# Performance work log

Hardware: AMD Instinct MI355X
Metric: run time of the kernel (lower is better)

## Reference

```python
import jax, jax.numpy as jnp
import numpy as np

D_MODEL = 1536
NUM_EXPERTS = 64
TOP_K = 2
D_HIDDEN = 512
LN_EPS = 1e-5


def setup_inputs() -> dict:
    key = jax.random.key(0)
    ks = jax.random.split(key, 6)
    B, S = 2, 2048
    x = jax.random.normal(ks[0], (B, S, D_MODEL), dtype=jnp.float32)
    # router: nn.Linear(d_model, num_experts, bias=False) -> weight [E, D]
    Wr = jax.random.normal(ks[1], (NUM_EXPERTS, D_MODEL), dtype=jnp.float32) / np.sqrt(D_MODEL)
    # per-expert MLP weights, torch Linear layout: w1 [H, D], w2 [D, H], stacked over experts
    W1 = jax.random.normal(ks[2], (NUM_EXPERTS, D_HIDDEN, D_MODEL), dtype=jnp.float32) / np.sqrt(D_MODEL)
    W2 = jax.random.normal(ks[3], (NUM_EXPERTS, D_MODEL, D_HIDDEN), dtype=jnp.float32) / np.sqrt(D_HIDDEN)
    gamma = jnp.ones((D_MODEL,), dtype=jnp.float32)
    beta = jnp.zeros((D_MODEL,), dtype=jnp.float32)
    return {"x": x, "Wr": Wr, "W1": W1, "W2": W2, "gamma": gamma, "beta": beta}


def reference(x, Wr, W1, W2, gamma, beta):
    B, S, D = x.shape
    xf = x.reshape(-1, D)                                   # [T, D]
    logits = xf @ Wr.T                                      # [T, E]
    top_w, top_idx = jax.lax.top_k(logits, TOP_K)           # [T, K]
    top_w = jax.nn.softmax(top_w, axis=-1)                  # softmax over selected k
    # combine[t, e] = sum_k top_w[t, k] * 1{top_idx[t,k]==e}; zero for unselected experts,
    # so dense all-expert compute below is mathematically identical to the masked loop.
    onehot = jax.nn.one_hot(top_idx, NUM_EXPERTS, dtype=xf.dtype)   # [T, K, E]
    combine = jnp.einsum("tk,tke->te", top_w, onehot)       # [T, E]
    h = jax.nn.silu(jnp.einsum("td,ehd->teh", xf, W1))      # [T, E, H]
    hw = h * combine[:, :, None]                            # weight before second GEMM
    out = jnp.einsum("teh,edh->td", hw, W2)                 # [T, D]
    # LayerNorm (eps=1e-5, affine)
    mu = jnp.mean(out, axis=-1, keepdims=True)
    var = jnp.mean(jnp.square(out - mu), axis=-1, keepdims=True)
    out = (out - mu) * jax.lax.rsqrt(var + LN_EPS) * gamma + beta
    return out.reshape(B, S, D)
```

## Files before the change

kernel.cpp:

```cpp
#include <hip/hip_runtime.h>
#include <hip/hip_bf16.h>

#define D_MODEL 1536
#define NEXP    64
#define D_HID   512
#define NTOK    4096
#define NT1     (D_MODEL / 64)
#define NT2     (D_HID / 64)
#define MT      192

typedef __attribute__((ext_vector_type(8))) short short8;
typedef __attribute__((ext_vector_type(4))) float f32x4;

__device__ __forceinline__ unsigned short f2bf(float f) {
  unsigned u = __builtin_bit_cast(unsigned, f);
  u += 0x7FFFu + ((u >> 16) & 1u);
  return (unsigned short)(u >> 16);
}
__device__ __forceinline__ unsigned pk2(float a, float b) {
  return (unsigned)f2bf(a) | ((unsigned)f2bf(b) << 16);
}
__device__ __forceinline__ float bf2f(unsigned short u) {
  return __builtin_bit_cast(float, ((unsigned)u) << 16);
}

__device__ __forceinline__ void gl16(const void* g, void* s) {
  __builtin_amdgcn_global_load_lds(
      (const __attribute__((address_space(1))) unsigned int*)g,
      (__attribute__((address_space(3))) unsigned int*)s, 16, 0, 0);
}

#define WAITV(N)  asm volatile("s_waitcnt vmcnt(" #N ")" ::: "memory")
#define WAITL0    asm volatile("s_waitcnt lgkmcnt(0)" ::: "memory")
#define SBAR      __builtin_amdgcn_s_barrier()
#define SCHED0    __builtin_amdgcn_sched_barrier(0)


__global__ void zero_small_kernel(int* __restrict__ counts) {
  counts[threadIdx.x] = 0;
}


__global__ __launch_bounds__(256) void cvt_split_kernel(const float* __restrict__ x,
    const float* __restrict__ Wr,
    unsigned short* __restrict__ xhi, unsigned short* __restrict__ xlo,
    unsigned short* __restrict__ whi, unsigned short* __restrict__ wlo)
{
  const float* src; unsigned short* dhi; unsigned short* dlo; long i;
  long bid = blockIdx.x;
  if (bid < 3072) { src = x;  dhi = xhi; dlo = xlo; i = (bid * 256 + threadIdx.x) * 8; }
  else            { src = Wr; dhi = whi; dlo = wlo; i = ((bid - 3072) * 256 + threadIdx.x) * 8; }
  float4 a = *(const float4*)(src + i);
  float4 b = *(const float4*)(src + i + 4);
  float f[8] = {a.x, a.y, a.z, a.w, b.x, b.y, b.z, b.w};
  unsigned short h[8], l[8];
  #pragma unroll
  for (int j = 0; j < 8; ++j) {
    h[j] = f2bf(f[j]);
    l[j] = f2bf(f[j] - bf2f(h[j]));
  }
  uint4 ph, pl;
  ph.x = (unsigned)h[0] | ((unsigned)h[1] << 16);
  ph.y = (unsigned)h[2] | ((unsigned)h[3] << 16);
  ph.z = (unsigned)h[4] | ((unsigned)h[5] << 16);
  ph.w = (unsigned)h[6] | ((unsigned)h[7] << 16);
  pl.x = (unsigned)l[0] | ((unsigned)l[1] << 16);
  pl.y = (unsigned)l[2] | ((unsigned)l[3] << 16);
  pl.z = (unsigned)l[4] | ((unsigned)l[5] << 16);
  pl.w = (unsigned)l[6] | ((unsigned)l[7] << 16);
  *(uint4*)(dhi + i) = ph;
  *(uint4*)(dlo + i) = pl;
}


__global__ __launch_bounds__(256) void router_kernel(
    const unsigned short* __restrict__ xhi, const unsigned short* __restrict__ xlo,
    const unsigned short* __restrict__ whi, const unsigned short* __restrict__ wlo,
    int* __restrict__ topidx, float* __restrict__ topw, int* __restrict__ counts)
{
  __shared__ unsigned short lds[8 * 4096];
  const int tid  = threadIdx.x;
  const int lane = tid & 63;
  const int wv   = tid >> 6;
  const int t0   = blockIdx.x * 64;

  const int lslot = (lane & 7) ^ (lane >> 3);
  const unsigned short* gsrc[4][2];
  #pragma unroll
  for (int j = 0; j < 2; ++j) {
    int r = (wv * 2 + j) * 8 + (lane >> 3);
    gsrc[0][j] = xhi + (long)(t0 + r) * D_MODEL + lslot * 8;
    gsrc[1][j] = xlo + (long)(t0 + r) * D_MODEL + lslot * 8;
    gsrc[2][j] = whi + (long)r * D_MODEL + lslot * 8;
    gsrc[3][j] = wlo + (long)r * D_MODEL + lslot * 8;
  }

  auto ISSUE = [&](int t, int b) {
    const int k0 = t * 64;
    SCHED0;
    #pragma unroll
    for (int tile = 0; tile < 4; ++tile)
      #pragma unroll
      for (int j = 0; j < 2; ++j)
        gl16(gsrc[tile][j] + k0, &lds[(b * 4 + tile) * 4096 + (wv * 2 + j) * 512]);
    SCHED0;
  };

  f32x4 acc[4];
  #pragma unroll
  for (int i = 0; i < 4; ++i) acc[i] = (f32x4)0.f;

  const int arow = wv * 16 + (lane & 15);

  auto COMPUTE = [&](int b) {
    const unsigned short* Ah = &lds[(b * 4 + 0) * 4096];
    const unsigned short* Al = &lds[(b * 4 + 1) * 4096];
    const unsigned short* Bh = &lds[(b * 4 + 2) * 4096];
    const unsigned short* Bl = &lds[(b * 4 + 3) * 4096];
    #pragma unroll
    for (int ks = 0; ks < 2; ++ks) {
      int pa = (ks * 4 + (lane >> 4)) ^ (arow & 7);
      short8 ah = *(const short8*)(Ah + arow * 64 + pa * 8);
      short8 al = *(const short8*)(Al + arow * 64 + pa * 8);
      short8 bh[4], bl[4];
      #pragma unroll
      for (int ni = 0; ni < 4; ++ni) {
        int br = ni * 16 + (lane & 15);
        int pb = (ks * 4 + (lane >> 4)) ^ (br & 7);
        bh[ni] = *(const short8*)(Bh + br * 64 + pb * 8);
        bl[ni] = *(const short8*)(Bl + br * 64 + pb * 8);
      }
      __builtin_amdgcn_s_setprio(1);
      #pragma unroll
      for (int ni = 0; ni < 4; ++ni) {
        acc[ni] = __builtin_amdgcn_mfma_f32_16x16x32_bf16(ah, bh[ni], acc[ni], 0, 0, 0);
        acc[ni] = __builtin_amdgcn_mfma_f32_16x16x32_bf16(ah, bl[ni], acc[ni], 0, 0, 0);
        acc[ni] = __builtin_amdgcn_mfma_f32_16x16x32_bf16(al, bh[ni], acc[ni], 0, 0, 0);
      }
      __builtin_amdgcn_s_setprio(0);
    }
  };

  ISSUE(0, 0);
  ISSUE(1, 1);
  WAITV(8);
  SBAR;

  #pragma unroll 1
  for (int t = 0; t < NT1; t += 2) {
    COMPUTE(0);
    SBAR;
    if (t + 2 < NT1) { ISSUE(t + 2, 0); WAITV(8); }
    else             { WAITV(0); }
    SBAR;
    COMPUTE(1);
    SBAR;
    if (t + 2 < NT1) {
      if (t + 3 < NT1) { ISSUE(t + 3, 1); WAITV(8); }
      else             { WAITV(0); }
      SBAR;
    }
  }

  float* lgl = (float*)lds;
  #pragma unroll
  for (int ni = 0; ni < 4; ++ni)
    #pragma unroll
    for (int rg = 0; rg < 4; ++rg) {
      int tok = wv * 16 + (lane >> 4) * 4 + rg;
      int e   = ni * 16 + (lane & 15);
      lgl[tok * 66 + e] = acc[ni][rg];
    }
  __syncthreads();

  for (int i = 0; i < 16; ++i) {
    const int tl = wv * 16 + i;
    float v = lgl[tl * 66 + lane];
    float v0 = v; int e0 = lane;
    #pragma unroll
    for (int off = 32; off > 0; off >>= 1) {
      float ov = __shfl_xor(v0, off);
      int   oe = __shfl_xor(e0, off);
      if (ov > v0 || (ov == v0 && oe < e0)) { v0 = ov; e0 = oe; }
    }
    float v1 = (lane == e0) ? -3.0e38f : v;
    int e1 = lane;
    #pragma unroll
    for (int off = 32; off > 0; off >>= 1) {
      float ov = __shfl_xor(v1, off);
      int   oe = __shfl_xor(e1, off);
      if (ov > v1 || (ov == v1 && oe < e1)) { v1 = ov; e1 = oe; }
    }
    if (lane == 0) {
      int tt = t0 + tl;
      float w0 = 1.f / (1.f + expf(v1 - v0));
      topidx[tt * 2]     = e0;
      topidx[tt * 2 + 1] = e1;
      topw[tt * 2]       = w0;
      topw[tt * 2 + 1]   = 1.f - w0;
      atomicAdd(&counts[e0], 1);
      atomicAdd(&counts[e1], 1);
    }
  }
}


__global__ void scan_kernel(const int* __restrict__ counts, int* __restrict__ offs,
                            int* __restrict__ cursor)
{
  int e = threadIdx.x;
  int c = counts[e];
  int xx = c;
  #pragma unroll
  for (int off = 1; off < 64; off <<= 1) {
    int y = __shfl_up(xx, off);
    if (e >= off) xx += y;
  }
  offs[e + 1] = xx;
  if (e == 0) offs[0] = 0;
  cursor[e] = 0;
}

__global__ void scatter_kernel(const int* __restrict__ topidx, const float* __restrict__ topw,
    const int* __restrict__ offs, int* __restrict__ cursor,
    int* __restrict__ perm, float* __restrict__ wgt, int* __restrict__ tok2slot)
{
  int t = blockIdx.x * blockDim.x + threadIdx.x;
  if (t >= NTOK) return;
  #pragma unroll
  for (int k = 0; k < 2; ++k) {
    int e = topidx[t * 2 + k];
    float w = topw[t * 2 + k];
    int pos = atomicAdd(&cursor[e], 1);
    int slot = offs[e] + pos;
    perm[slot] = t;
    wgt[slot] = w;
    tok2slot[t * 2 + k] = slot;
  }
}


__global__ __launch_bounds__(256, 2) void ffn1_kernel(
    const unsigned short* __restrict__ xb, const float* __restrict__ W1,
    const int* __restrict__ offs, const int* __restrict__ perm,
    const float* __restrict__ wgt, unsigned short* __restrict__ hbuf)
{
  const int nc = blockIdx.x;
  const int e  = blockIdx.y;
  const int cnt = offs[e + 1] - offs[e];
  if (cnt == 0) return;

  __shared__ unsigned short Abuf[2][MT * 64];
  __shared__ unsigned short Bbuf[2][64 * 64];

  const int tid  = threadIdx.x;
  const int lane = tid & 63;
  const int wv   = tid >> 6;

  const int qB = tid & 15;
  const int rB = tid >> 4;
  const float* bptr[4];
  #pragma unroll
  for (int p = 0; p < 4; ++p)
    bptr[p] = W1 + ((long)e * D_HID + nc * 64 + p * 16 + rB) * D_MODEL + qB * 4;

  int arow[3], brow[4];
  int physA[2][3], physB[2][4];
  #pragma unroll
  for (int mi = 0; mi < 3; ++mi) {
    arow[mi] = wv * 48 + mi * 16 + (lane & 15);
    #pragma unroll
    for (int ks = 0; ks < 2; ++ks)
      physA[ks][mi] = (ks * 4 + (lane >> 4)) ^ (arow[mi] & 7);
  }
  #pragma unroll
  for (int ni = 0; ni < 4; ++ni) {
    brow[ni] = ni * 16 + (lane & 15);
    #pragma unroll
    for (int ks = 0; ks < 2; ++ks)
      physB[ks][ni] = (ks * 4 + (lane >> 4)) ^ (brow[ni] & 7);
  }
  const int lslot = (lane & 7) ^ (lane >> 3);

  for (int m0 = 0; m0 < cnt; m0 += MT) {
    const int base = offs[e] + m0;
    const int mcnt = min(MT, cnt - m0);

    const unsigned short* gptrA[6];
    #pragma unroll
    for (int j = 0; j < 6; ++j) {
      int pr = (wv * 6 + j) * 8 + (lane >> 3);
      if (pr >= mcnt) pr = mcnt - 1;
      gptrA[j] = xb + (long)perm[base + pr] * D_MODEL + lslot * 8;
    }

    f32x4 acc[3][4];
    #pragma unroll
    for (int i = 0; i < 3; ++i)
      #pragma unroll
      for (int j = 0; j < 4; ++j) acc[i][j] = (f32x4)0.f;

    float4 bregA[4], bregB[4];

    auto ISSUE = [&](int t, float4* br, unsigned short* Ab) {
      const int k0 = t * 64;
      SCHED0;
      #pragma unroll
      for (int p = 0; p < 4; ++p) br[p] = *(const float4*)(bptr[p] + k0);
      SCHED0;
      #pragma unroll
      for (int j = 0; j < 6; ++j)
        gl16(gptrA[j] + k0, Ab + (wv * 6 + j) * 512);
      SCHED0;
    };
    auto WRITE_B = [&](const float4* br, unsigned short* B_) {
      #pragma unroll
      for (int p = 0; p < 4; ++p) {
        int rr = p * 16 + rB;
        unsigned lo = pk2(br[p].x, br[p].y);
        unsigned hi = pk2(br[p].z, br[p].w);
        int ph = (qB >> 1) ^ (rr & 7);
        *(uint2*)(B_ + rr * 64 + ph * 8 + (qB & 1) * 4) = make_uint2(lo, hi);
      }
    };
    auto COMPUTE = [&](const unsigned short* A_, const unsigned short* B_) {
      #pragma unroll
      for (int ks = 0; ks < 2; ++ks) {
        short8 a[3], bb[4];
        #pragma unroll
        for (int mi = 0; mi < 3; ++mi)
          a[mi] = *(const short8*)(A_ + arow[mi] * 64 + physA[ks][mi] * 8);
        #pragma unroll
        for (int ni = 0; ni < 4; ++ni)
          bb[ni] = *(const short8*)(B_ + brow[ni] * 64 + physB[ks][ni] * 8);
        __builtin_amdgcn_s_setprio(1);
        #pragma unroll
        for (int mi = 0; mi < 3; ++mi)
          #pragma unroll
          for (int ni = 0; ni < 4; ++ni)
            acc[mi][ni] = __builtin_amdgcn_mfma_f32_16x16x32_bf16(a[mi], bb[ni], acc[mi][ni], 0, 0, 0);
        __builtin_amdgcn_s_setprio(0);
      }
    };

    ISSUE(0, bregA, Abuf[0]);
    WAITV(6);
    WRITE_B(bregA, Bbuf[0]);
    ISSUE(1, bregB, Abuf[1]);
    WAITV(10);
    WAITL0;
    SBAR;

    #pragma unroll 1
    for (int t = 0; t < NT1; t += 2) {
      COMPUTE(Abuf[0], Bbuf[0]);
      SBAR;
      WAITV(6);
      WRITE_B(bregB, Bbuf[1]);
      if (t + 2 < NT1) { ISSUE(t + 2, bregA, Abuf[0]); WAITV(10); }
      else             { WAITV(0); }
      WAITL0;
      SBAR;
      COMPUTE(Abuf[1], Bbuf[1]);
      SBAR;
      if (t + 2 < NT1) {
        WAITV(6);
        WRITE_B(bregA, Bbuf[0]);
        if (t + 3 < NT1) { ISSUE(t + 3, bregB, Abuf[1]); WAITV(10); }
        else             { WAITV(0); }
        WAITL0;
        SBAR;
      }
    }

    unsigned short* fds = &Abuf[0][0];
    const int rsub = (lane >> 4) * 4;
    const int csub = lane & 15;
    #pragma unroll
    for (int mi = 0; mi < 3; ++mi) {
      #pragma unroll
      for (int rg = 0; rg < 4; ++rg) {
        int r = wv * 48 + mi * 16 + rsub + rg;
        float wt = (r < mcnt) ? wgt[base + r] : 0.f;
        #pragma unroll
        for (int ni = 0; ni < 4; ++ni) {
          float v = acc[mi][ni][rg];
          float sv = v / (1.f + __expf(-v)) * wt;
          fds[r * 64 + ni * 16 + csub] = f2bf(sv);
        }
      }
    }
    __syncthreads();
    #pragma unroll
    for (int q = 0; q < 6; ++q) {
      int idx = q * 256 + tid;
      int row = idx >> 3, c8 = idx & 7;
      if (row < mcnt)
        *(uint4*)(hbuf + (long)(base + row) * D_HID + nc * 64 + c8 * 8) =
            *(const uint4*)(fds + row * 64 + c8 * 8);
    }
    __syncthreads();
  }
}


__global__ __launch_bounds__(256, 2) void ffn2_kernel(
    const unsigned short* __restrict__ hbuf, const float* __restrict__ W2,
    const int* __restrict__ offs, unsigned short* __restrict__ sbuf)
{
  const int nc = blockIdx.x;
  const int e  = blockIdx.y;
  const int cnt = offs[e + 1] - offs[e];
  if (cnt == 0) return;

  __shared__ unsigned short Abuf[2][MT * 64];
  __shared__ unsigned short Bbuf[2][64 * 64];

  const int tid  = threadIdx.x;
  const int lane = tid & 63;
  const int wv   = tid >> 6;

  const int qB = tid & 15;
  const int rB = tid >> 4;
  const float* bptr[4];
  #pragma unroll
  for (int p = 0; p < 4; ++p)
    bptr[p] = W2 + ((long)e * D_MODEL + nc * 64 + p * 16 + rB) * D_HID + qB * 4;

  int arow[3], brow[4];
  int physA[2][3], physB[2][4];
  #pragma unroll
  for (int mi = 0; mi < 3; ++mi) {
    arow[mi] = wv * 48 + mi * 16 + (lane & 15);
    #pragma unroll
    for (int ks = 0; ks < 2; ++ks)
      physA[ks][mi] = (ks * 4 + (lane >> 4)) ^ (arow[mi] & 7);
  }
  #pragma unroll
  for (int ni = 0; ni < 4; ++ni) {
    brow[ni] = ni * 16 + (lane & 15);
    #pragma unroll
    for (int ks = 0; ks < 2; ++ks)
      physB[ks][ni] = (ks * 4 + (lane >> 4)) ^ (brow[ni] & 7);
  }
  const int lslot = (lane & 7) ^ (lane >> 3);

  for (int m0 = 0; m0 < cnt; m0 += MT) {
    const int base = offs[e] + m0;
    const int mcnt = min(MT, cnt - m0);

    const unsigned short* gptrA[6];
    #pragma unroll
    for (int j = 0; j < 6; ++j) {
      int pr = (wv * 6 + j) * 8 + (lane >> 3);
      if (pr >= mcnt) pr = mcnt - 1;
      gptrA[j] = hbuf + (long)(base + pr) * D_HID + lslot * 8;
    }

    f32x4 acc[3][4];
    #pragma unroll
    for (int i = 0; i < 3; ++i)
      #pragma unroll
      for (int j = 0; j < 4; ++j) acc[i][j] = (f32x4)0.f;

    float4 bregA[4], bregB[4];

    auto ISSUE = [&](int t, float4* br, unsigned short* Ab) {
      const int k0 = t * 64;
      SCHED0;
      #pragma unroll
      for (int p = 0; p < 4; ++p) br[p] = *(const float4*)(bptr[p] + k0);
      SCHED0;
      #pragma unroll
      for (int j = 0; j < 6; ++j)
        gl16(gptrA[j] + k0, Ab + (wv * 6 + j) * 512);
      SCHED0;
    };
    auto WRITE_B = [&](const float4* br, unsigned short* B_) {
      #pragma unroll
      for (int p = 0; p < 4; ++p) {
        int rr = p * 16 + rB;
        unsigned lo = pk2(br[p].x, br[p].y);
        unsigned hi = pk2(br[p].z, br[p].w);
        int ph = (qB >> 1) ^ (rr & 7);
        *(uint2*)(B_ + rr * 64 + ph * 8 + (qB & 1) * 4) = make_uint2(lo, hi);
      }
    };
    auto COMPUTE = [&](const unsigned short* A_, const unsigned short* B_) {
      #pragma unroll
      for (int ks = 0; ks < 2; ++ks) {
        short8 a[3], bb[4];
        #pragma unroll
        for (int mi = 0; mi < 3; ++mi)
          a[mi] = *(const short8*)(A_ + arow[mi] * 64 + physA[ks][mi] * 8);
        #pragma unroll
        for (int ni = 0; ni < 4; ++ni)
          bb[ni] = *(const short8*)(B_ + brow[ni] * 64 + physB[ks][ni] * 8);
        __builtin_amdgcn_s_setprio(1);
        #pragma unroll
        for (int mi = 0; mi < 3; ++mi)
          #pragma unroll
          for (int ni = 0; ni < 4; ++ni)
            acc[mi][ni] = __builtin_amdgcn_mfma_f32_16x16x32_bf16(a[mi], bb[ni], acc[mi][ni], 0, 0, 0);
        __builtin_amdgcn_s_setprio(0);
      }
    };

    ISSUE(0, bregA, Abuf[0]);
    WAITV(6);
    WRITE_B(bregA, Bbuf[0]);
    ISSUE(1, bregB, Abuf[1]);
    WAITV(10);
    WAITL0;
    SBAR;

    #pragma unroll 1
    for (int t = 0; t < NT2; t += 2) {
      COMPUTE(Abuf[0], Bbuf[0]);
      SBAR;
      WAITV(6);
      WRITE_B(bregB, Bbuf[1]);
      if (t + 2 < NT2) { ISSUE(t + 2, bregA, Abuf[0]); WAITV(10); }
      else             { WAITV(0); }
      WAITL0;
      SBAR;
      COMPUTE(Abuf[1], Bbuf[1]);
      SBAR;
      if (t + 2 < NT2) {
        WAITV(6);
        WRITE_B(bregA, Bbuf[0]);
        if (t + 3 < NT2) { ISSUE(t + 3, bregB, Abuf[1]); WAITV(10); }
        else             { WAITV(0); }
        WAITL0;
        SBAR;
      }
    }

    unsigned short* fds = &Abuf[0][0];
    const int rsub = (lane >> 4) * 4;
    const int csub = lane & 15;
    #pragma unroll
    for (int mi = 0; mi < 3; ++mi) {
      #pragma unroll
      for (int rg = 0; rg < 4; ++rg) {
        int r = wv * 48 + mi * 16 + rsub + rg;
        #pragma unroll
        for (int ni = 0; ni < 4; ++ni)
          fds[r * 64 + ni * 16 + csub] = f2bf(acc[mi][ni][rg]);
      }
    }
    __syncthreads();
    #pragma unroll
    for (int q = 0; q < 6; ++q) {
      int idx = q * 256 + tid;
      int row = idx >> 3, c8 = idx & 7;
      if (row < mcnt)
        *(uint4*)(sbuf + (long)(base + row) * D_MODEL + nc * 64 + c8 * 8) =
            *(const uint4*)(fds + row * 64 + c8 * 8);
    }
    __syncthreads();
  }
}


__global__ __launch_bounds__(192) void ln_kernel(const unsigned short* __restrict__ sbuf,
    const int* __restrict__ tok2slot, float* __restrict__ out,
    const float* __restrict__ gamma, const float* __restrict__ beta)
{
  const int tid = threadIdx.x;
  const int t = blockIdx.x;
  const long r0 = (long)tok2slot[t * 2]     * D_MODEL;
  const long r1 = (long)tok2slot[t * 2 + 1] * D_MODEL;

  uint4 u0 = *(const uint4*)(sbuf + r0 + tid * 8);
  uint4 u1 = *(const uint4*)(sbuf + r1 + tid * 8);
  float v[8];
  {
    const unsigned* p0 = &u0.x;
    const unsigned* p1 = &u1.x;
    #pragma unroll
    for (int i = 0; i < 4; ++i) {
      v[i * 2]     = bf2f((unsigned short)(p0[i] & 0xFFFFu)) + bf2f((unsigned short)(p1[i] & 0xFFFFu));
      v[i * 2 + 1] = bf2f((unsigned short)(p0[i] >> 16))     + bf2f((unsigned short)(p1[i] >> 16));
    }
  }

  float s = 0.f, sq = 0.f;
  #pragma unroll
  for (int i = 0; i < 8; ++i) { s += v[i]; sq += v[i] * v[i]; }
  #pragma unroll
  for (int off = 32; off > 0; off >>= 1) {
    s  += __shfl_xor(s, off);
    sq += __shfl_xor(sq, off);
  }
  __shared__ float ss[3], sqs[3];
  int wv = tid >> 6;
  if ((tid & 63) == 0) { ss[wv] = s; sqs[wv] = sq; }
  __syncthreads();
  s  = ss[0] + ss[1] + ss[2];
  sq = sqs[0] + sqs[1] + sqs[2];
  const float inv = 1.f / (float)D_MODEL;
  float mu  = s * inv;
  float var = sq * inv - mu * mu;
  float rs  = 1.f / sqrtf(var + 1e-5f);

  float4 g1 = *(const float4*)(gamma + tid * 8);
  float4 g2 = *(const float4*)(gamma + tid * 8 + 4);
  float4 b1v = *(const float4*)(beta + tid * 8);
  float4 b2v = *(const float4*)(beta + tid * 8 + 4);
  float4 a, b;
  a.x = (v[0] - mu) * rs * g1.x + b1v.x;
  a.y = (v[1] - mu) * rs * g1.y + b1v.y;
  a.z = (v[2] - mu) * rs * g1.z + b1v.z;
  a.w = (v[3] - mu) * rs * g1.w + b1v.w;
  b.x = (v[4] - mu) * rs * g2.x + b2v.x;
  b.y = (v[5] - mu) * rs * g2.y + b2v.y;
  b.z = (v[6] - mu) * rs * g2.z + b2v.z;
  b.w = (v[7] - mu) * rs * g2.w + b2v.w;
  float* row = out + (long)t * D_MODEL;
  *(float4*)(row + tid * 8)     = a;
  *(float4*)(row + tid * 8 + 4) = b;
}


extern "C" void kernel_launch(void* const* d_in, const int* in_sizes, int n_in,
                              void* d_out, int out_size, void* d_ws, size_t ws_size,
                              hipStream_t stream) {
  const float* x     = (const float*)d_in[0];
  const float* Wr    = (const float*)d_in[1];
  const float* W1    = (const float*)d_in[2];
  const float* W2    = (const float*)d_in[3];
  const float* gamma = (const float*)d_in[4];
  const float* beta  = (const float*)d_in[5];
  float* out = (float*)d_out;

  char* ws = (char*)d_ws;
  unsigned short* xhi    = (unsigned short*)(ws + 0);
  unsigned short* xlo    = (unsigned short*)(ws + 12582912);
  unsigned short* hbuf   = (unsigned short*)(ws + 25165824);
  unsigned short* sbuf   = (unsigned short*)(ws + 33554432);
  unsigned short* whi    = (unsigned short*)(ws + 58720256);
  unsigned short* wlo    = (unsigned short*)(ws + 58916864);
  int*   topidx   = (int*)  (ws + 59113472);
  float* topw     = (float*)(ws + 59146240);
  int*   counts   = (int*)  (ws + 59179008);
  int*   cursor   = (int*)  (ws + 59179264);
  int*   offs     = (int*)  (ws + 59179520);
  int*   tok2slot = (int*)  (ws + 59180032);
  int*   perm     = (int*)  (ws + 59212800);
  float* wgt      = (float*)(ws + 59245568);

  hipLaunchKernelGGL(zero_small_kernel, dim3(1), dim3(64), 0, stream, counts);
  hipLaunchKernelGGL(cvt_split_kernel, dim3(3120), dim3(256), 0, stream, x, Wr, xhi, xlo, whi, wlo);
  hipLaunchKernelGGL(router_kernel, dim3(NTOK / 64), dim3(256), 0, stream, xhi, xlo, whi, wlo, topidx, topw, counts);
  hipLaunchKernelGGL(scan_kernel, dim3(1), dim3(64), 0, stream, counts, offs, cursor);
  hipLaunchKernelGGL(scatter_kernel, dim3(NTOK / 256), dim3(256), 0, stream, topidx, topw, offs, cursor, perm, wgt, tok2slot);
  hipLaunchKernelGGL(ffn1_kernel, dim3(8, NEXP), dim3(256), 0, stream, xhi, W1, offs, perm, wgt, hbuf);
  hipLaunchKernelGGL(ffn2_kernel, dim3(24, NEXP), dim3(256), 0, stream, hbuf, W2, offs, sbuf);
  hipLaunchKernelGGL(ln_kernel, dim3(NTOK), dim3(192), 0, stream, sbuf, tok2slot, out, gamma, beta);
}
```

Baseline: 217.9 us.

## Deepen B-operand prefetch to three register stages in expert FFN GEMMs

New measurement: 220.6 us. About the same (+1.2%).

```diff
diff --git a/kernel.cpp b/kernel.cpp
--- a/kernel.cpp
+++ b/kernel.cpp
@@ -239,6 +239,19 @@
   }
 }
 
+#define FS(T, AB, BRI, BRW, KNT)                                   \
+  {                                                                \
+    COMPUTE(Abuf[AB], Bbuf[AB]);                                   \
+    SBAR;                                                          \
+    if ((T) + 2 < (KNT)) ISSUEA((T) + 2, Abuf[AB]);                \
+    if ((T) + 3 < (KNT)) ISSUEB((T) + 3, BRI);                     \
+    if ((T) + 3 < (KNT))      { WAITV(14); }                       \
+    else if ((T) + 2 < (KNT)) { WAITV(10); }                       \
+    else                      { WAITV(0);  }                       \
+    if ((T) + 1 < (KNT)) { WRITE_B(BRW, Bbuf[(AB) ^ 1]); WAITL0; } \
+    SBAR;                                                          \
+  }
+
 
 __global__ __launch_bounds__(256, 2) void ffn1_kernel(
     const unsigned short* __restrict__ xb, const float* __restrict__ W1,
@@ -300,17 +313,21 @@
       #pragma unroll
       for (int j = 0; j < 4; ++j) acc[i][j] = (f32x4)0.f;
 
-    float4 bregA[4], bregB[4];
-
-    auto ISSUE = [&](int t, float4* br, unsigned short* Ab) {
+    float4 br0[4], br1[4], br2[4];
+
+    auto ISSUEA = [&](int t, unsigned short* Ab) {
       const int k0 = t * 64;
-      SCHED0;
-      #pragma unroll
-      for (int p = 0; p < 4; ++p) br[p] = *(const float4*)(bptr[p] + k0);
       SCHED0;
       #pragma unroll
       for (int j = 0; j < 6; ++j)
         gl16(gptrA[j] + k0, Ab + (wv * 6 + j) * 512);
+      SCHED0;
+    };
+    auto ISSUEB = [&](int t, float4* br) {
+      const int k0 = t * 64;
+      SCHED0;
+      #pragma unroll
+      for (int p = 0; p < 4; ++p) br[p] = *(const float4*)(bptr[p] + k0);
       SCHED0;
     };
     auto WRITE_B = [&](const float4* br, unsigned short* B_) {
@@ -343,34 +360,22 @@
       }
     };
 
-    ISSUE(0, bregA, Abuf[0]);
-    WAITV(6);
-    WRITE_B(bregA, Bbuf[0]);
-    ISSUE(1, bregB, Abuf[1]);
-    WAITV(10);
+    ISSUEA(0, Abuf[0]); ISSUEB(0, br0);
+    ISSUEA(1, Abuf[1]); ISSUEB(1, br1);
+    ISSUEB(2, br2);
+    WAITV(14);
+    WRITE_B(br0, Bbuf[0]);
     WAITL0;
     SBAR;
 
     #pragma unroll 1
-    for (int t = 0; t < NT1; t += 2) {
-      COMPUTE(Abuf[0], Bbuf[0]);
-      SBAR;
-      WAITV(6);
-      WRITE_B(bregB, Bbuf[1]);
-      if (t + 2 < NT1) { ISSUE(t + 2, bregA, Abuf[0]); WAITV(10); }
-      else             { WAITV(0); }
-      WAITL0;
-      SBAR;
-      COMPUTE(Abuf[1], Bbuf[1]);
-      SBAR;
-      if (t + 2 < NT1) {
-        WAITV(6);
-        WRITE_B(bregA, Bbuf[0]);
-        if (t + 3 < NT1) { ISSUE(t + 3, bregB, Abuf[1]); WAITV(10); }
-        else             { WAITV(0); }
-        WAITL0;
-        SBAR;
-      }
+    for (int t = 0; t < NT1; t += 6) {
+      FS(t + 0, 0, br0, br1, NT1);
+      FS(t + 1, 1, br1, br2, NT1);
+      FS(t + 2, 0, br2, br0, NT1);
+      FS(t + 3, 1, br0, br1, NT1);
+      FS(t + 4, 0, br1, br2, NT1);
+      FS(t + 5, 1, br2, br0, NT1);
     }
 
     unsigned short* fds = &Abuf[0][0];
@@ -463,17 +468,21 @@
       #pragma unroll
       for (int j = 0; j < 4; ++j) acc[i][j] = (f32x4)0.f;
 
-    float4 bregA[4], bregB[4];
-
-    auto ISSUE = [&](int t, float4* br, unsigned short* Ab) {
+    float4 br0[4], br1[4], br2[4];
+
+    auto ISSUEA = [&](int t, unsigned short* Ab) {
       const int k0 = t * 64;
-      SCHED0;
-      #pragma unroll
-      for (int p = 0; p < 4; ++p) br[p] = *(const float4*)(bptr[p] + k0);
       SCHED0;
       #pragma unroll
       for (int j = 0; j < 6; ++j)
         gl16(gptrA[j] + k0, Ab + (wv * 6 + j) * 512);
+      SCHED0;
+    };
+    auto ISSUEB = [&](int t, float4* br) {
+      const int k0 = t * 64;
+      SCHED0;
+      #pragma unroll
+      for (int p = 0; p < 4; ++p) br[p] = *(const float4*)(bptr[p] + k0);
       SCHED0;
     };
     auto WRITE_B = [&](const float4* br, unsigned short* B_) {
@@ -506,35 +515,22 @@
       }
     };
 
-    ISSUE(0, bregA, Abuf[0]);
-    WAITV(6);
-    WRITE_B(bregA, Bbuf[0]);
-    ISSUE(1, bregB, Abuf[1]);
-    WAITV(10);
+    ISSUEA(0, Abuf[0]); ISSUEB(0, br0);
+    ISSUEA(1, Abuf[1]); ISSUEB(1, br1);
+    ISSUEB(2, br2);
+    WAITV(14);
+    WRITE_B(br0, Bbuf[0]);
     WAITL0;
     SBAR;
 
-    #pragma unroll 1
-    for (int t = 0; t < NT2; t += 2) {
-      COMPUTE(Abuf[0], Bbuf[0]);
-      SBAR;
-      WAITV(6);
-      WRITE_B(bregB, Bbuf[1]);
-      if (t + 2 < NT2) { ISSUE(t + 2, bregA, Abuf[0]); WAITV(10); }
-      else             { WAITV(0); }
-      WAITL0;
-      SBAR;
-      COMPUTE(Abuf[1], Bbuf[1]);
-      SBAR;
-      if (t + 2 < NT2) {
-        WAITV(6);
-        WRITE_B(bregA, Bbuf[0]);
-        if (t + 3 < NT2) { ISSUE(t + 3, bregB, Abuf[1]); WAITV(10); }
-        else             { WAITV(0); }
-        WAITL0;
-        SBAR;
-      }
-    }
+    FS(0, 0, br0, br1, NT2);
+    FS(1, 1, br1, br2, NT2);
+    FS(2, 0, br2, br0, NT2);
+    FS(3, 1, br0, br1, NT2);
+    FS(4, 0, br1, br2, NT2);
+    FS(5, 1, br2, br0, NT2);
+    FS(6, 0, br0, br1, NT2);
+    FS(7, 1, br1, br2, NT2);
 
     unsigned short* fds = &Abuf[0][0];
     const int rsub = (lane >> 4) * 4;
```
